# Performance work log

Measured on AMD Instinct MI355X. Metric: run time of the kernel, lower is better.

## Reference

```python
import jax, jax.numpy as jnp
import numpy as np

N_HEADS = 16


def setup_inputs() -> dict:
    key = jax.random.key(0)
    ks = jax.random.split(key, 9)
    B, S, D = 2, 2048, 2048
    s = 0.02
    return {
        "X": jax.random.normal(ks[0], (B, S, D), jnp.float32),
        "Wq": jax.random.normal(ks[1], (D, D), jnp.float32) * s,
        "bq": jax.random.normal(ks[2], (D,), jnp.float32) * s,
        "Wk": jax.random.normal(ks[3], (D, D), jnp.float32) * s,
        "bk": jax.random.normal(ks[4], (D,), jnp.float32) * s,
        "Wv": jax.random.normal(ks[5], (D, D), jnp.float32) * s,
        "bv": jax.random.normal(ks[6], (D,), jnp.float32) * s,
        "Wo": jax.random.normal(ks[7], (D, D), jnp.float32) * s,
        "bo": jax.random.normal(ks[8], (D,), jnp.float32) * s,
    }


def reference(X, Wq, bq, Wk, bk, Wv, bv, Wo, bo):
    B, S, D = X.shape
    H = N_HEADS
    d_head = D // H
    # qk_scale = 1/sqrt(sqrt(d_head)), applied to BOTH Q and K
    scale = jnp.asarray(1.0 / np.sqrt(np.sqrt(d_head)), X.dtype)
    Q = (X @ Wq.T + bq).reshape(B, S, H, d_head) * scale  # bqhd
    K = (X @ Wk.T + bk).reshape(B, S, H, d_head) * scale  # bkhd
    V = (X @ Wv.T + bv).reshape(B, S, H, d_head)          # bkhd
    scores = jnp.einsum("bqhd,bkhd->bhqk", Q, K)
    causal = jnp.tril(jnp.ones((S, S), bool))  # [q, k]
    scores = jnp.where(causal[None, None], scores, -jnp.inf)
    # original casts logits to fp32 before softmax, back to Q dtype after
    attn = jax.nn.softmax(scores.astype(jnp.float32), axis=-1).astype(X.dtype)
    out = jnp.einsum("bhqk,bkhd->bqhd", attn, V).reshape(B, S, D)
    return out @ Wo.T + bo
```

## Files before the change

### kernel.cpp

```cpp
#include <hip/hip_runtime.h>


typedef __attribute__((ext_vector_type(8))) short bfx8;
typedef __attribute__((ext_vector_type(4))) float f32x4;

#define TO_GLOBAL(p) ((const __attribute__((address_space(1))) void*)(p))
#define TO_LDS(p)    ((__attribute__((address_space(3))) void*)(p))

__device__ __forceinline__ unsigned short f2bf(float f) {
    unsigned int u = __float_as_uint(f);
    u += 0x7FFFu + ((u >> 16) & 1u);
    return (unsigned short)(u >> 16);
}

__device__ __forceinline__ void store_out(unsigned short* p, float v) { *p = f2bf(v); }
__device__ __forceinline__ void store_out(float* p, float v) { *p = v; }

__global__ void cast_bf16_kernel(const float* __restrict__ x,
                                 unsigned short* __restrict__ y, int n4) {
    int i = blockIdx.x * blockDim.x + threadIdx.x;
    int st = gridDim.x * blockDim.x;
    for (; i < n4; i += st) {
        float4 v = reinterpret_cast<const float4*>(x)[i];
        ushort4 o;
        o.x = f2bf(v.x); o.y = f2bf(v.y); o.z = f2bf(v.z); o.w = f2bf(v.w);
        reinterpret_cast<ushort4*>(y)[i] = o;
    }
}

template <typename OUT>
__global__ __launch_bounds__(256) void gemm_bt(
    const unsigned short* __restrict__ A, const unsigned short* __restrict__ Bw,
    const float* __restrict__ bias, OUT* __restrict__ C,
    int M, int N, int K, float scale) {
    __shared__ __align__(16) unsigned short Ash[128 * 32];
    __shared__ __align__(16) unsigned short Bsh[128 * 32];

    const int tid  = threadIdx.x;
    const int lane = tid & 63;
    const int w    = tid >> 6;
    const int g    = lane >> 4;
    const int l15  = lane & 15;
    const int m0   = blockIdx.y * 128;
    const int n0   = blockIdx.x * 128;
    const int wm   = (w >> 1) * 64;
    const int wn   = (w & 1) * 64;

    f32x4 acc[4][4];
#pragma unroll
    for (int i = 0; i < 4; i++)
#pragma unroll
        for (int j = 0; j < 4; j++) acc[i][j] = (f32x4){0.f, 0.f, 0.f, 0.f};

    const int c0 = tid, c1 = tid + 256;
    const int rowA0 = c0 >> 2, colA0 = (c0 & 3) * 8;
    const int rowA1 = c1 >> 2, colA1 = (c1 & 3) * 8;

    for (int k0 = 0; k0 < K; k0 += 32) {
        __syncthreads();
        __builtin_amdgcn_global_load_lds(TO_GLOBAL(A + (size_t)(m0 + rowA0) * K + k0 + colA0),
                                         TO_LDS(&Ash[c0 * 8]), 16, 0, 0);
        __builtin_amdgcn_global_load_lds(TO_GLOBAL(A + (size_t)(m0 + rowA1) * K + k0 + colA1),
                                         TO_LDS(&Ash[c1 * 8]), 16, 0, 0);
        __builtin_amdgcn_global_load_lds(TO_GLOBAL(Bw + (size_t)(n0 + rowA0) * K + k0 + colA0),
                                         TO_LDS(&Bsh[c0 * 8]), 16, 0, 0);
        __builtin_amdgcn_global_load_lds(TO_GLOBAL(Bw + (size_t)(n0 + rowA1) * K + k0 + colA1),
                                         TO_LDS(&Bsh[c1 * 8]), 16, 0, 0);
        __syncthreads();

        bfx8 af[4], bfr[4];
#pragma unroll
        for (int mi = 0; mi < 4; mi++)
            af[mi] = *reinterpret_cast<const bfx8*>(&Ash[(wm + mi * 16 + l15) * 32 + g * 8]);
#pragma unroll
        for (int ni = 0; ni < 4; ni++)
            bfr[ni] = *reinterpret_cast<const bfx8*>(&Bsh[(wn + ni * 16 + l15) * 32 + g * 8]);
#pragma unroll
        for (int mi = 0; mi < 4; mi++)
#pragma unroll
            for (int ni = 0; ni < 4; ni++)
                acc[mi][ni] = __builtin_amdgcn_mfma_f32_16x16x32_bf16(af[mi], bfr[ni],
                                                                     acc[mi][ni], 0, 0, 0);
    }

#pragma unroll
    for (int mi = 0; mi < 4; mi++) {
#pragma unroll
        for (int ni = 0; ni < 4; ni++) {
            const int col = n0 + wn + ni * 16 + l15;
            const float bv = bias[col];
#pragma unroll
            for (int r = 0; r < 4; r++) {
                const int row = m0 + wm + mi * 16 + g * 4 + r;
                store_out(&C[(size_t)row * N + col], (acc[mi][ni][r] + bv) * scale);
            }
        }
    }
}

__global__ __launch_bounds__(256) void transpose_v(const unsigned short* __restrict__ V,
                                                   unsigned short* __restrict__ Vt) {
    __shared__ unsigned short tile[64][72];
    const int tid = threadIdx.x;
    const int r0 = blockIdx.y * 64;
    const int c0 = blockIdx.x * 64;
    const int b = r0 >> 11, sbase = r0 & 2047;
#pragma unroll
    for (int i = 0; i < 2; i++) {
        const int row = tid >> 2;
        const int ch  = (tid & 3) + 4 * i;
        bfx8 v = *reinterpret_cast<const bfx8*>(V + (size_t)(r0 + row) * 2048 + c0 + ch * 8);
        *reinterpret_cast<bfx8*>(&tile[row][ch * 8]) = v;
    }
    __syncthreads();
    const int dh  = tid & 63;
    const int s_l = (tid >> 6) * 16;
    unsigned short* dst = Vt + (size_t)(b * 2048 + c0 + dh) * 2048 + sbase + s_l;
#pragma unroll
    for (int half = 0; half < 2; half++) {
        bfx8 o;
#pragma unroll
        for (int j = 0; j < 8; j++) o[j] = (short)tile[s_l + half * 8 + j][dh];
        *reinterpret_cast<bfx8*>(dst + half * 8) = o;
    }
}

#define SLEN 2048
#define DMODEL 2048
#define M2FIX 11.541560327f

__global__ __launch_bounds__(256) void attn_kernel(
    const unsigned short* __restrict__ Q, const unsigned short* __restrict__ Kp,
    const unsigned short* __restrict__ Vt, unsigned short* __restrict__ O) {
    __shared__ __align__(16) unsigned short Ksh[2][64 * 128];
    __shared__ __align__(16) unsigned short Vsh[2][128 * 64];
    __shared__ __align__(16) unsigned short Psh[4 * 1024];

    const int tid  = threadIdx.x;
    const int lane = tid & 63;
    const int w    = tid >> 6;
    const int g    = lane >> 4;
    const int l15  = lane & 15;
    const int bh   = blockIdx.x;
    const int b    = bh >> 4, h = bh & 15;
    const int pr   = blockIdx.y;

    const size_t bhbase = (size_t)b * SLEN * DMODEL + (size_t)h * 128;
    const size_t vtbase = (size_t)bh * 128 * SLEN;

    unsigned short* Pw = &Psh[w * 1024];
    const int khi_b = l15 >> 3, klo = l15 & 7;
    const int vsw = l15 & 7;

    const int krow = tid >> 4, kch = tid & 15;
    const int vdr  = tid >> 3, vch = tid & 7;

    int cur = 0;

#define STAGE(BUF, KB)                                                              \
    {                                                                               \
        _Pragma("unroll")                                                           \
        for (int i_ = 0; i_ < 4; i_++) {                                            \
            const int row_ = krow + 16 * i_;                                        \
            __builtin_amdgcn_global_load_lds(                                       \
                TO_GLOBAL(Kp + bhbase + (size_t)((KB) + row_) * DMODEL +            \
                          ((kch ^ (row_ & 7)) * 8)),                                \
                TO_LDS(&Ksh[BUF][(tid + 256 * i_) * 8]), 16, 0, 0);                 \
        }                                                                           \
        _Pragma("unroll")                                                           \
        for (int i_ = 0; i_ < 4; i_++) {                                            \
            const int dr_ = vdr + 32 * i_;                                          \
            __builtin_amdgcn_global_load_lds(                                       \
                TO_GLOBAL(Vt + vtbase + (size_t)dr_ * SLEN + (KB) +                 \
                          ((vch ^ (dr_ & 7)) * 8)),                                 \
                TO_LDS(&Vsh[BUF][(tid + 256 * i_) * 8]), 16, 0, 0);                 \
        }                                                                           \
    }

#pragma unroll 1
    for (int seg = 0; seg < 2; seg++) {
        const int qt  = seg == 0 ? (31 - pr) : pr;
        const int q0w = qt * 64 + w * 16;

        bfx8 qf[4];
#pragma unroll
        for (int c = 0; c < 4; c++)
            qf[c] = *reinterpret_cast<const bfx8*>(
                Q + bhbase + (size_t)(q0w + l15) * DMODEL + c * 32 + g * 8);

        f32x4 oacc[8];
#pragma unroll
        for (int i = 0; i < 8; i++) oacc[i] = (f32x4){0.f, 0.f, 0.f, 0.f};
        float lpart[4] = {0.f, 0.f, 0.f, 0.f};

        const int ntile = qt + 1;
        STAGE(cur, 0);

#pragma unroll 1
        for (int t = 0; t < ntile; t++) {
            const int kb = t * 64;
            __builtin_amdgcn_s_barrier();
            if (t + 1 < ntile) {
                STAGE(cur ^ 1, kb + 64);
                asm volatile("s_waitcnt vmcnt(8)" ::: "memory");
            } else {
                asm volatile("s_waitcnt vmcnt(0)" ::: "memory");
            }
            __builtin_amdgcn_s_barrier();

            const unsigned short* Kb_ = &Ksh[cur][0];
            const unsigned short* Vb_ = &Vsh[cur][0];
            f32x4 sacc[4];
#pragma unroll
            for (int kt = 0; kt < 4; kt++) sacc[kt] = (f32x4){0.f, 0.f, 0.f, 0.f};
#pragma unroll
            for (int kt = 0; kt < 4; kt++) {
                const int row = kt * 16 + l15;
#pragma unroll
                for (int c = 0; c < 4; c++) {
                    bfx8 kf = *reinterpret_cast<const bfx8*>(
                        &Kb_[row * 128 + (((c * 4 + g) ^ (row & 7)) * 8)]);
                    sacc[kt] = __builtin_amdgcn_mfma_f32_16x16x32_bf16(
                        qf[c], kf, sacc[kt], 0, 0, 0);
                }
            }
            if (t == ntile - 1) {
#pragma unroll
                for (int kt = 0; kt < 4; kt++)
#pragma unroll
                    for (int r = 0; r < 4; r++)
                        if (kb + kt * 16 + l15 > q0w + g * 4 + r)
                            sacc[kt][r] = -1e30f;
            }
#pragma unroll
            for (int r = 0; r < 4; r++) {
                const float p0 = exp2f(sacc[0][r] - M2FIX);
                const float p1 = exp2f(sacc[1][r] - M2FIX);
                const float p2 = exp2f(sacc[2][r] - M2FIX);
                const float p3 = exp2f(sacc[3][r] - M2FIX);
                lpart[r] += (p0 + p1) + (p2 + p3);
                const int ql = g * 4 + r;
                const int swz = ql & 7;
                Pw[ql * 64 + (((khi_b + 0) ^ swz) << 3) + klo] = f2bf(p0);
                Pw[ql * 64 + (((khi_b + 2) ^ swz) << 3) + klo] = f2bf(p1);
                Pw[ql * 64 + (((khi_b + 4) ^ swz) << 3) + klo] = f2bf(p2);
                Pw[ql * 64 + (((khi_b + 6) ^ swz) << 3) + klo] = f2bf(p3);
            }
#pragma unroll
            for (int ks = 0; ks < 2; ks++) {
                bfx8 vb[8];
#pragma unroll
                for (int ni = 0; ni < 8; ni++) {
                    const int d = ni * 16 + l15;
                    vb[ni] = *reinterpret_cast<const bfx8*>(
                        &Vb_[d * 64 + (((ks * 4 + g) ^ vsw) * 8)]);
                }
                bfx8 pa = *reinterpret_cast<const bfx8*>(
                    Pw + l15 * 64 + (((ks * 4 + g) ^ vsw) << 3));
#pragma unroll
                for (int ni = 0; ni < 8; ni++)
                    oacc[ni] = __builtin_amdgcn_mfma_f32_16x16x32_bf16(
                        pa, vb[ni], oacc[ni], 0, 0, 0);
            }
            cur ^= 1;
        }

#pragma unroll
        for (int r = 0; r < 4; r++) {
            float l = lpart[r];
#pragma unroll
            for (int s = 1; s < 16; s <<= 1) l += __shfl_xor(l, s);
            const float inv = 1.0f / l;
            const int q = q0w + g * 4 + r;
#pragma unroll
            for (int ni = 0; ni < 8; ni++)
                O[bhbase + (size_t)q * DMODEL + ni * 16 + l15] = f2bf(oacc[ni][r] * inv);
        }
    }
#undef STAGE
}

extern "C" void kernel_launch(void* const* d_in, const int* in_sizes, int n_in,
                              void* d_out, int out_size, void* d_ws, size_t ws_size,
                              hipStream_t stream) {
    const float* X  = (const float*)d_in[0];
    const float* Wq = (const float*)d_in[1];
    const float* bq = (const float*)d_in[2];
    const float* Wk = (const float*)d_in[3];
    const float* bk = (const float*)d_in[4];
    const float* Wv = (const float*)d_in[5];
    const float* bv = (const float*)d_in[6];
    const float* Wo = (const float*)d_in[7];
    const float* bo = (const float*)d_in[8];
    float* out = (float*)d_out;

    unsigned short* ws  = (unsigned short*)d_ws;
    unsigned short* Qb  = ws;
    unsigned short* Kb  = ws + 8388608;
    unsigned short* Vtb = ws + 16777216;
    unsigned short* XOb = ws + 25165824;
    unsigned short* Wb  = ws + 33554432;
    unsigned short* Vstage = (unsigned short*)d_out;

    const float qk_scale = 0.35709585f;

    const dim3 cb(256);
    const dim3 gg(16, 32), gb(256);

    cast_bf16_kernel<<<dim3(2048), cb, 0, stream>>>(X, XOb, 2097152);

    cast_bf16_kernel<<<dim3(1024), cb, 0, stream>>>(Wq, Wb, 1048576);
    gemm_bt<unsigned short><<<gg, gb, 0, stream>>>(XOb, Wb, bq, Qb, 4096, 2048, 2048, qk_scale);

    cast_bf16_kernel<<<dim3(1024), cb, 0, stream>>>(Wk, Wb, 1048576);
    gemm_bt<unsigned short><<<gg, gb, 0, stream>>>(XOb, Wb, bk, Kb, 4096, 2048, 2048, qk_scale);

    cast_bf16_kernel<<<dim3(1024), cb, 0, stream>>>(Wv, Wb, 1048576);
    gemm_bt<unsigned short><<<gg, gb, 0, stream>>>(XOb, Wb, bv, Vstage, 4096, 2048, 2048, 1.0f);
    transpose_v<<<dim3(32, 64), cb, 0, stream>>>(Vstage, Vtb);

    attn_kernel<<<dim3(32, 16), gb, 0, stream>>>(Qb, Kb, Vtb, XOb);

    cast_bf16_kernel<<<dim3(1024), cb, 0, stream>>>(Wo, Wb, 1048576);
    gemm_bt<float><<<gg, gb, 0, stream>>>(XOb, Wb, bo, out, 4096, 2048, 2048, 1.0f);
}
```

Before: 324.6 us.

## Batch QKV projections into one launch and register-stage attention K/V tiles

The three weight casts become one kernel and the three QKV GEMMs become one launch with a z-dimension, so each launch fills the GPU with more blocks and the serial small launches go away. The attention kernel drops its double-buffered LDS staging through global_load_lds and instead prefetches the next K/V tile into registers, then writes it into a single LDS buffer each iteration. It also sets launch bounds for 3 waves per SIMD and raises wave priority around the MFMA sections. The register prefetch halves LDS use to allow more resident blocks, but it adds register pressure and an extra LDS write and barrier on every tile.

```diff
diff --git a/kernel.cpp b/kernel.cpp
--- a/kernel.cpp
+++ b/kernel.cpp
@@ -25,6 +25,22 @@
         ushort4 o;
         o.x = f2bf(v.x); o.y = f2bf(v.y); o.z = f2bf(v.z); o.w = f2bf(v.w);
         reinterpret_cast<ushort4*>(y)[i] = o;
+    }
+}
+
+__global__ void cast3_kernel(const float* __restrict__ s0, const float* __restrict__ s1,
+                             const float* __restrict__ s2,
+                             unsigned short* __restrict__ d0, unsigned short* __restrict__ d1,
+                             unsigned short* __restrict__ d2, int n4) {
+    const float* s = (blockIdx.y == 0) ? s0 : (blockIdx.y == 1) ? s1 : s2;
+    unsigned short* d = (blockIdx.y == 0) ? d0 : (blockIdx.y == 1) ? d1 : d2;
+    int i = blockIdx.x * blockDim.x + threadIdx.x;
+    int st = gridDim.x * blockDim.x;
+    for (; i < n4; i += st) {
+        float4 v = reinterpret_cast<const float4*>(s)[i];
+        ushort4 o;
+        o.x = f2bf(v.x); o.y = f2bf(v.y); o.z = f2bf(v.z); o.w = f2bf(v.w);
+        reinterpret_cast<ushort4*>(d)[i] = o;
     }
 }
 
@@ -98,6 +114,86 @@
     }
 }
 
+__global__ __launch_bounds__(256) void gemm_qkv(
+    const unsigned short* __restrict__ A,
+    const unsigned short* __restrict__ W0, const unsigned short* __restrict__ W1,
+    const unsigned short* __restrict__ W2,
+    const float* __restrict__ b0, const float* __restrict__ b1,
+    const float* __restrict__ b2,
+    unsigned short* __restrict__ C0, unsigned short* __restrict__ C1,
+    unsigned short* __restrict__ C2, float qks) {
+    const int z = blockIdx.z;
+    const unsigned short* Bw = (z == 0) ? W0 : (z == 1) ? W1 : W2;
+    const float* bias = (z == 0) ? b0 : (z == 1) ? b1 : b2;
+    unsigned short* C = (z == 0) ? C0 : (z == 1) ? C1 : C2;
+    const float scale = (z < 2) ? qks : 1.0f;
+    const int M = 4096, N = 2048, K = 2048;
+
+    __shared__ __align__(16) unsigned short Ash[128 * 32];
+    __shared__ __align__(16) unsigned short Bsh[128 * 32];
+
+    const int tid  = threadIdx.x;
+    const int lane = tid & 63;
+    const int w    = tid >> 6;
+    const int g    = lane >> 4;
+    const int l15  = lane & 15;
+    const int m0   = blockIdx.y * 128;
+    const int n0   = blockIdx.x * 128;
+    const int wm   = (w >> 1) * 64;
+    const int wn   = (w & 1) * 64;
+
+    f32x4 acc[4][4];
+#pragma unroll
+    for (int i = 0; i < 4; i++)
+#pragma unroll
+        for (int j = 0; j < 4; j++) acc[i][j] = (f32x4){0.f, 0.f, 0.f, 0.f};
+
+    const int c0 = tid, c1 = tid + 256;
+    const int rowA0 = c0 >> 2, colA0 = (c0 & 3) * 8;
+    const int rowA1 = c1 >> 2, colA1 = (c1 & 3) * 8;
+
+    for (int k0 = 0; k0 < K; k0 += 32) {
+        __syncthreads();
+        __builtin_amdgcn_global_load_lds(TO_GLOBAL(A + (size_t)(m0 + rowA0) * K + k0 + colA0),
+                                         TO_LDS(&Ash[c0 * 8]), 16, 0, 0);
+        __builtin_amdgcn_global_load_lds(TO_GLOBAL(A + (size_t)(m0 + rowA1) * K + k0 + colA1),
+                                         TO_LDS(&Ash[c1 * 8]), 16, 0, 0);
+        __builtin_amdgcn_global_load_lds(TO_GLOBAL(Bw + (size_t)(n0 + rowA0) * K + k0 + colA0),
+                                         TO_LDS(&Bsh[c0 * 8]), 16, 0, 0);
+        __builtin_amdgcn_global_load_lds(TO_GLOBAL(Bw + (size_t)(n0 + rowA1) * K + k0 + colA1),
+                                         TO_LDS(&Bsh[c1 * 8]), 16, 0, 0);
+        __syncthreads();
+
+        bfx8 af[4], bfr[4];
+#pragma unroll
+        for (int mi = 0; mi < 4; mi++)
+            af[mi] = *reinterpret_cast<const bfx8*>(&Ash[(wm + mi * 16 + l15) * 32 + g * 8]);
+#pragma unroll
+        for (int ni = 0; ni < 4; ni++)
+            bfr[ni] = *reinterpret_cast<const bfx8*>(&Bsh[(wn + ni * 16 + l15) * 32 + g * 8]);
+#pragma unroll
+        for (int mi = 0; mi < 4; mi++)
+#pragma unroll
+            for (int ni = 0; ni < 4; ni++)
+                acc[mi][ni] = __builtin_amdgcn_mfma_f32_16x16x32_bf16(af[mi], bfr[ni],
+                                                                     acc[mi][ni], 0, 0, 0);
+    }
+
+#pragma unroll
+    for (int mi = 0; mi < 4; mi++) {
+#pragma unroll
+        for (int ni = 0; ni < 4; ni++) {
+            const int col = n0 + wn + ni * 16 + l15;
+            const float bv = bias[col];
+#pragma unroll
+            for (int r = 0; r < 4; r++) {
+                const int row = m0 + wm + mi * 16 + g * 4 + r;
+                C[(size_t)row * N + col] = f2bf((acc[mi][ni][r] + bv) * scale);
+            }
+        }
+    }
+}
+
 __global__ __launch_bounds__(256) void transpose_v(const unsigned short* __restrict__ V,
                                                    unsigned short* __restrict__ Vt) {
     __shared__ unsigned short tile[64][72];
@@ -129,11 +225,11 @@
 #define DMODEL 2048
 #define M2FIX 11.541560327f
 
-__global__ __launch_bounds__(256) void attn_kernel(
+__global__ __launch_bounds__(256, 3) void attn_kernel(
     const unsigned short* __restrict__ Q, const unsigned short* __restrict__ Kp,
     const unsigned short* __restrict__ Vt, unsigned short* __restrict__ O) {
-    __shared__ __align__(16) unsigned short Ksh[2][64 * 128];
-    __shared__ __align__(16) unsigned short Vsh[2][128 * 64];
+    __shared__ __align__(16) unsigned short Ksh[64 * 128];
+    __shared__ __align__(16) unsigned short Vsh[128 * 64];
     __shared__ __align__(16) unsigned short Psh[4 * 1024];
 
     const int tid  = threadIdx.x;
@@ -155,26 +251,18 @@
     const int krow = tid >> 4, kch = tid & 15;
     const int vdr  = tid >> 3, vch = tid & 7;
 
-    int cur = 0;
-
-#define STAGE(BUF, KB)                                                              \
+    bfx8 kreg[4], vreg[4];
+
+#define LOADREGS(KB)                                                                \
     {                                                                               \
         _Pragma("unroll")                                                           \
-        for (int i_ = 0; i_ < 4; i_++) {                                            \
-            const int row_ = krow + 16 * i_;                                        \
-            __builtin_amdgcn_global_load_lds(                                       \
-                TO_GLOBAL(Kp + bhbase + (size_t)((KB) + row_) * DMODEL +            \
-                          ((kch ^ (row_ & 7)) * 8)),                                \
-                TO_LDS(&Ksh[BUF][(tid + 256 * i_) * 8]), 16, 0, 0);                 \
-        }                                                                           \
+        for (int i_ = 0; i_ < 4; i_++)                                              \
+            kreg[i_] = *reinterpret_cast<const bfx8*>(                              \
+                Kp + bhbase + (size_t)((KB) + krow + 16 * i_) * DMODEL + kch * 8);  \
         _Pragma("unroll")                                                           \
-        for (int i_ = 0; i_ < 4; i_++) {                                            \
-            const int dr_ = vdr + 32 * i_;                                          \
-            __builtin_amdgcn_global_load_lds(                                       \
-                TO_GLOBAL(Vt + vtbase + (size_t)dr_ * SLEN + (KB) +                 \
-                          ((vch ^ (dr_ & 7)) * 8)),                                 \
-                TO_LDS(&Vsh[BUF][(tid + 256 * i_) * 8]), 16, 0, 0);                 \
-        }                                                                           \
+        for (int i_ = 0; i_ < 4; i_++)                                              \
+            vreg[i_] = *reinterpret_cast<const bfx8*>(                              \
+                Vt + vtbase + (size_t)(vdr + 32 * i_) * SLEN + (KB) + vch * 8);     \
     }
 
 #pragma unroll 1
@@ -194,22 +282,29 @@
         float lpart[4] = {0.f, 0.f, 0.f, 0.f};
 
         const int ntile = qt + 1;
-        STAGE(cur, 0);
+        LOADREGS(0);
 
 #pragma unroll 1
         for (int t = 0; t < ntile; t++) {
             const int kb = t * 64;
             __builtin_amdgcn_s_barrier();
-            if (t + 1 < ntile) {
-                STAGE(cur ^ 1, kb + 64);
-                asm volatile("s_waitcnt vmcnt(8)" ::: "memory");
-            } else {
-                asm volatile("s_waitcnt vmcnt(0)" ::: "memory");
-            }
+            __builtin_amdgcn_sched_barrier(0);
+#pragma unroll
+            for (int i = 0; i < 4; i++) {
+                const int row = krow + 16 * i;
+                *reinterpret_cast<bfx8*>(&Ksh[row * 128 + ((kch ^ (row & 7)) * 8)]) = kreg[i];
+            }
+#pragma unroll
+            for (int i = 0; i < 4; i++) {
+                const int dr = vdr + 32 * i;
+                *reinterpret_cast<bfx8*>(&Vsh[dr * 64 + ((vch ^ (dr & 7)) * 8)]) = vreg[i];
+            }
+            asm volatile("s_waitcnt lgkmcnt(0)" ::: "memory");
             __builtin_amdgcn_s_barrier();
-
-            const unsigned short* Kb_ = &Ksh[cur][0];
-            const unsigned short* Vb_ = &Vsh[cur][0];
+            __builtin_amdgcn_sched_barrier(0);
+            if (t + 1 < ntile) LOADREGS(kb + 64);
+
+            __builtin_amdgcn_s_setprio(1);
             f32x4 sacc[4];
 #pragma unroll
             for (int kt = 0; kt < 4; kt++) sacc[kt] = (f32x4){0.f, 0.f, 0.f, 0.f};
@@ -219,11 +314,12 @@
 #pragma unroll
                 for (int c = 0; c < 4; c++) {
                     bfx8 kf = *reinterpret_cast<const bfx8*>(
-                        &Kb_[row * 128 + (((c * 4 + g) ^ (row & 7)) * 8)]);
+                        &Ksh[row * 128 + (((c * 4 + g) ^ (row & 7)) * 8)]);
                     sacc[kt] = __builtin_amdgcn_mfma_f32_16x16x32_bf16(
                         qf[c], kf, sacc[kt], 0, 0, 0);
                 }
             }
+            __builtin_amdgcn_s_setprio(0);
             if (t == ntile - 1) {
 #pragma unroll
                 for (int kt = 0; kt < 4; kt++)
@@ -246,6 +342,7 @@
                 Pw[ql * 64 + (((khi_b + 4) ^ swz) << 3) + klo] = f2bf(p2);
                 Pw[ql * 64 + (((khi_b + 6) ^ swz) << 3) + klo] = f2bf(p3);
             }
+            __builtin_amdgcn_s_setprio(1);
 #pragma unroll
             for (int ks = 0; ks < 2; ks++) {
                 bfx8 vb[8];
@@ -253,7 +350,7 @@
                 for (int ni = 0; ni < 8; ni++) {
                     const int d = ni * 16 + l15;
                     vb[ni] = *reinterpret_cast<const bfx8*>(
-                        &Vb_[d * 64 + (((ks * 4 + g) ^ vsw) * 8)]);
+                        &Vsh[d * 64 + (((ks * 4 + g) ^ vsw) * 8)]);
                 }
                 bfx8 pa = *reinterpret_cast<const bfx8*>(
                     Pw + l15 * 64 + (((ks * 4 + g) ^ vsw) << 3));
@@ -262,7 +359,7 @@
                     oacc[ni] = __builtin_amdgcn_mfma_f32_16x16x32_bf16(
                         pa, vb[ni], oacc[ni], 0, 0, 0);
             }
-            cur ^= 1;
+            __builtin_amdgcn_s_setprio(0);
         }
 
 #pragma unroll
@@ -277,7 +374,7 @@
                 O[bhbase + (size_t)q * DMODEL + ni * 16 + l15] = f2bf(oacc[ni][r] * inv);
         }
     }
-#undef STAGE
+#undef LOADREGS
 }
 
 extern "C" void kernel_launch(void* const* d_in, const int* in_sizes, int n_in,
@@ -300,27 +397,25 @@
     unsigned short* Vtb = ws + 16777216;
     unsigned short* XOb = ws + 25165824;
     unsigned short* Wb  = ws + 33554432;
-    unsigned short* Vstage = (unsigned short*)d_out;
+    unsigned short* out_u   = (unsigned short*)d_out;
+    unsigned short* Vstage  = out_u;
+    unsigned short* Wkb     = out_u + 8388608;
+    unsigned short* Wvb     = out_u + 12582912;
 
     const float qk_scale = 0.35709585f;
 
     const dim3 cb(256);
-    const dim3 gg(16, 32), gb(256);
 
     cast_bf16_kernel<<<dim3(2048), cb, 0, stream>>>(X, XOb, 2097152);
-
-    cast_bf16_kernel<<<dim3(1024), cb, 0, stream>>>(Wq, Wb, 1048576);
-    gemm_bt<unsigned short><<<gg, gb, 0, stream>>>(XOb, Wb, bq, Qb, 4096, 2048, 2048, qk_scale);
-
-    cast_bf16_kernel<<<dim3(1024), cb, 0, stream>>>(Wk, Wb, 1048576);
-    gemm_bt<unsigned short><<<gg, gb, 0, stream>>>(XOb, Wb, bk, Kb, 4096, 2048, 2048, qk_scale);
-
-    cast_bf16_kernel<<<dim3(1024), cb, 0, stream>>>(Wv, Wb, 1048576);
-    gemm_bt<unsigned short><<<gg, gb, 0, stream>>>(XOb, Wb, bv, Vstage, 4096, 2048, 2048, 1.0f);
+    cast3_kernel<<<dim3(1024, 3), cb, 0, stream>>>(Wq, Wk, Wv, Wb, Wkb, Wvb, 1048576);
+
+    gemm_qkv<<<dim3(16, 32, 3), cb, 0, stream>>>(XOb, Wb, Wkb, Wvb, bq, bk, bv,
+                                                 Qb, Kb, Vstage, qk_scale);
+
     transpose_v<<<dim3(32, 64), cb, 0, stream>>>(Vstage, Vtb);
 
-    attn_kernel<<<dim3(32, 16), gb, 0, stream>>>(Qb, Kb, Vtb, XOb);
+    attn_kernel<<<dim3(32, 16), cb, 0, stream>>>(Qb, Kb, Vtb, XOb);
 
     cast_bf16_kernel<<<dim3(1024), cb, 0, stream>>>(Wo, Wb, 1048576);
-    gemm_bt<float><<<gg, gb, 0, stream>>>(XOb, Wb, bo, out, 4096, 2048, 2048, 1.0f);
-}
+    gemm_bt<float><<<dim3(16, 32), cb, 0, stream>>>(XOb, Wb, bo, out, 4096, 2048, 2048, 1.0f);
+}
```

New measurement: 282.5 us. 13.0% less time.
